# Optimization experiments

Measured on AMD Instinct MI355X. Metric: run time of the kernel, lower is better.

Reference implementation:

```python
import jax, jax.numpy as jnp
import numpy as np

B, S, D = 8, 4, 2048
H, HD = 32, 64
CACHE = 4096


def setup_inputs() -> dict:
    key = jax.random.key(0)
    ks = jax.random.split(key, 8)
    x = jax.random.normal(ks[0], (B, S, D), jnp.float32)
    # rotary frequencies for absolute positions CACHE..CACHE+S-1 (decode step)
    pos = np.arange(CACHE, CACHE + S, dtype=np.float64)[:, None]
    inv = 1.0 / (10000.0 ** (np.arange(0, HD, 2, dtype=np.float64) / HD))
    ang = pos * inv[None, :]
    freqs_cos = jnp.asarray(np.cos(ang), jnp.float32)  # [S, HD//2]
    freqs_sin = jnp.asarray(np.sin(ang), jnp.float32)
    total = CACHE + S
    m = np.zeros((1, 1, S, total), np.float32)
    m[0, 0, :, CACHE:] = np.triu(np.full((S, S), -1e9, np.float32), 1)
    mask = jnp.asarray(m)
    cache_k = jax.random.normal(ks[1], (B, CACHE, H, HD), jnp.float32)
    cache_v = jax.random.normal(ks[2], (B, CACHE, H, HD), jnp.float32)
    scale = 0.02
    wq = scale * jax.random.normal(ks[3], (D, D), jnp.float32)
    wk = scale * jax.random.normal(ks[4], (D, D), jnp.float32)
    wv = scale * jax.random.normal(ks[5], (D, D), jnp.float32)
    wo = scale * jax.random.normal(ks[6], (D, D), jnp.float32)
    return {"x": x, "freqs_cos": freqs_cos, "freqs_sin": freqs_sin,
            "mask": mask, "cache_k": cache_k, "cache_v": cache_v,
            "wq": wq, "wk": wk, "wv": wv, "wo": wo, "start_pos": CACHE}


def _rope(t, cos, sin):
    # t: [B, S, H, HD]; rotate consecutive pairs (complex multiply by e^{i*theta})
    b, s, h, hd = t.shape
    tr = t.reshape(b, s, h, hd // 2, 2)
    t0, t1 = tr[..., 0], tr[..., 1]
    c = cos[None, :, None, :]
    sn = sin[None, :, None, :]
    o0 = t0 * c - t1 * sn
    o1 = t0 * sn + t1 * c
    return jnp.stack([o0, o1], axis=-1).reshape(b, s, h, hd)


def reference(x, freqs_cos, freqs_sin, mask, cache_k, cache_v, wq, wk, wv, wo, start_pos):
    b, s, d = x.shape
    # torch Linear: y = x @ W.T
    xq = (x @ wq.T).reshape(b, s, H, HD)
    xk = (x @ wk.T).reshape(b, s, H, HD)
    xv = (x @ wv.T).reshape(b, s, H, HD)
    xq = _rope(xq, freqs_cos, freqs_sin)
    xk = _rope(xk, freqs_cos, freqs_sin)
    keys = jnp.concatenate([cache_k, xk], axis=1)    # [B, CACHE+S, H, HD]
    values = jnp.concatenate([cache_v, xv], axis=1)
    scale = 1.0 / jnp.sqrt(jnp.asarray(HD, x.dtype))
    scores = jnp.einsum('bqhd,bkhd->bhqk', xq, keys) * scale
    scores = jax.nn.softmax(scores + mask, axis=-1)
    out = jnp.einsum('bhqk,bkhd->bqhd', scores, values).reshape(b, s, d)
    return out @ wo.T
```

## Files before the change

kernel.cpp:

```cpp
#include <hip/hip_runtime.h>

#define DD     2048
#define MM     32
#define HH     32
#define HDIM   64
#define NCACHE 4096
#define KSPLIT 16
#define KR     128
#define NTILE  64
#define LSTR   132

__global__ __launch_bounds__(256) void gemm_partial_k(
    const float* __restrict__ A,
    const float* __restrict__ W0, const float* __restrict__ W1, const float* __restrict__ W2,
    float* __restrict__ partial)
{
    __shared__ float xs[MM][LSTR];
    __shared__ float wsh[NTILE][LSTR];
    const int nt = blockIdx.x, ks = blockIdx.y, wsel = blockIdx.z;
    const float* W = (wsel == 0) ? W0 : (wsel == 1 ? W1 : W2);
    const int k0 = ks * KR, n0 = nt * NTILE, t = threadIdx.x;

#pragma unroll
    for (int p = 0; p < 4; ++p) {
        int idx = t + 256 * p, row = idx >> 5, c4 = (idx & 31) << 2;
        *(float4*)&xs[row][c4] = *(const float4*)(A + (size_t)row * DD + k0 + c4);
    }
#pragma unroll
    for (int p = 0; p < 8; ++p) {
        int idx = t + 256 * p, row = idx >> 5, c4 = (idx & 31) << 2;
        *(float4*)&wsh[row][c4] = *(const float4*)(W + (size_t)(n0 + row) * DD + k0 + c4);
    }
    __syncthreads();

    const int np = t & 31;
    const int m0 = (t >> 5) << 2;
    float acc[4][2] = {{0.f,0.f},{0.f,0.f},{0.f,0.f},{0.f,0.f}};
#pragma unroll 4
    for (int kk = 0; kk < KR; kk += 4) {
        float4 w0 = *(float4*)&wsh[np][kk];
        float4 w1 = *(float4*)&wsh[np + 32][kk];
#pragma unroll
        for (int i = 0; i < 4; ++i) {
            float4 xv = *(float4*)&xs[m0 + i][kk];
            acc[i][0] += xv.x * w0.x + xv.y * w0.y + xv.z * w0.z + xv.w * w0.w;
            acc[i][1] += xv.x * w1.x + xv.y * w1.y + xv.z * w1.z + xv.w * w1.w;
        }
    }
    float* outp = partial + (size_t)(wsel * KSPLIT + ks) * MM * DD;
#pragma unroll
    for (int i = 0; i < 4; ++i) {
        outp[(size_t)(m0 + i) * DD + n0 + np]      = acc[i][0];
        outp[(size_t)(m0 + i) * DD + n0 + 32 + np] = acc[i][1];
    }
}

__global__ __launch_bounds__(256) void reduce_rope_k(
    const float* __restrict__ partial,
    const float* __restrict__ fc, const float* __restrict__ fs,
    float* __restrict__ qkv)
{
    int tid  = blockIdx.x * 256 + threadIdx.x;
    int wsel = tid >> 15;
    int r    = tid & 32767;
    int m    = r >> 10;
    int pr   = r & 1023;
    int n0   = pr << 1;

    const float* p = partial + (size_t)wsel * KSPLIT * MM * DD + (size_t)m * DD + n0;
    float e0 = 0.f, e1 = 0.f;
#pragma unroll
    for (int ksp = 0; ksp < KSPLIT; ++ksp) {
        float2 v = *(const float2*)(p + (size_t)ksp * MM * DD);
        e0 += v.x; e1 += v.y;
    }
    if (wsel < 2) {
        int s = m & 3;
        int i = (n0 & 63) >> 1;
        float c = fc[s * 32 + i], sn = fs[s * 32 + i];
        float o0 = e0 * c - e1 * sn;
        float o1 = e0 * sn + e1 * c;
        e0 = o0; e1 = o1;
    }
    float2 o; o.x = e0; o.y = e1;
    *(float2*)(qkv + (size_t)wsel * MM * DD + (size_t)m * DD + n0) = o;
}

__global__ __launch_bounds__(1024, 4) void attn_k(
    const float* __restrict__ cache_k, const float* __restrict__ cache_v,
    const float* __restrict__ qkv, float* __restrict__ attn_out)
{
    const int b = blockIdx.x >> 5, h = blockIdx.x & 31;
    const int t = threadIdx.x, lane16 = t & 15, grp = t >> 4;
    const int e0 = lane16 << 2;

    float4 q4[4];
#pragma unroll
    for (int q = 0; q < 4; ++q)
        q4[q] = *(const float4*)(qkv + (size_t)(b * 4 + q) * DD + h * HDIM + e0);

    float  l[4]   = {0.f, 0.f, 0.f, 0.f};
    float4 acc[4];
#pragma unroll
    for (int q = 0; q < 4; ++q) { acc[q].x = acc[q].y = acc[q].z = acc[q].w = 0.f; }

    const size_t pstride = (size_t)HH * HDIM;
    const float* kb = cache_k + ((size_t)b * NCACHE * HH + h) * HDIM + e0;
    const float* vb = cache_v + ((size_t)b * NCACHE * HH + h) * HDIM + e0;

    float4 kv = *(const float4*)(kb + (size_t)grp * pstride);
    float4 vv = *(const float4*)(vb + (size_t)grp * pstride);

    for (int it = 0; it < 64; ++it) {
        int pn = grp + (it + 1) * 64;
        if (pn > NCACHE - 1) pn = grp;
        float4 kn = *(const float4*)(kb + (size_t)pn * pstride);
        float4 vn = *(const float4*)(vb + (size_t)pn * pstride);
#pragma unroll
        for (int q = 0; q < 4; ++q) {
            float d = q4[q].x * kv.x + q4[q].y * kv.y + q4[q].z * kv.z + q4[q].w * kv.w;
            d += __shfl_xor(d, 1);
            d += __shfl_xor(d, 2);
            d += __shfl_xor(d, 4);
            d += __shfl_xor(d, 8);
            float pexp = __expf(d * 0.125f);
            l[q] += pexp;
            acc[q].x += pexp * vv.x;
            acc[q].y += pexp * vv.y;
            acc[q].z += pexp * vv.z;
            acc[q].w += pexp * vv.w;
        }
        kv = kn; vv = vn;
    }

    if (grp < 4) {
        const int j = grp;
        float4 k2 = *(const float4*)(qkv + (size_t)MM * DD + (size_t)(b * 4 + j) * DD + h * HDIM + e0);
        float4 v2 = *(const float4*)(qkv + (size_t)2 * MM * DD + (size_t)(b * 4 + j) * DD + h * HDIM + e0);
#pragma unroll
        for (int q = 0; q < 4; ++q) {
            float d = q4[q].x * k2.x + q4[q].y * k2.y + q4[q].z * k2.z + q4[q].w * k2.w;
            d += __shfl_xor(d, 1);
            d += __shfl_xor(d, 2);
            d += __shfl_xor(d, 4);
            d += __shfl_xor(d, 8);
            if (j <= q) {
                float pexp = __expf(d * 0.125f);
                l[q] += pexp;
                acc[q].x += pexp * v2.x;
                acc[q].y += pexp * v2.y;
                acc[q].z += pexp * v2.z;
                acc[q].w += pexp * v2.w;
            }
        }
    }

#pragma unroll
    for (int ofs = 16; ofs < 64; ofs <<= 1) {
#pragma unroll
        for (int q = 0; q < 4; ++q) {
            l[q]     += __shfl_xor(l[q], ofs);
            acc[q].x += __shfl_xor(acc[q].x, ofs);
            acc[q].y += __shfl_xor(acc[q].y, ofs);
            acc[q].z += __shfl_xor(acc[q].z, ofs);
            acc[q].w += __shfl_xor(acc[q].w, ofs);
        }
    }

    __shared__ float lacc[16][4][64];
    __shared__ float lsum[16][4];
    const int w = t >> 6;
    if ((t & 63) < 16) {
#pragma unroll
        for (int q = 0; q < 4; ++q)
            *(float4*)&lacc[w][q][e0] = acc[q];
        if (lane16 == 0) {
#pragma unroll
            for (int q = 0; q < 4; ++q) lsum[w][q] = l[q];
        }
    }
    __syncthreads();
    if (t < 256) {
        int q = t >> 6, e = t & 63;
        float s = 0.f, lt = 0.f;
#pragma unroll
        for (int w2 = 0; w2 < 16; ++w2) { s += lacc[w2][q][e]; lt += lsum[w2][q]; }
        attn_out[(size_t)(b * 4 + q) * DD + h * HDIM + e] = s / lt;
    }
}

__global__ __launch_bounds__(256) void reduce_out_k(
    const float* __restrict__ partial, float* __restrict__ out)
{
    int tid = blockIdx.x * 256 + threadIdx.x;
    int n0 = tid << 1;
    float e0 = 0.f, e1 = 0.f;
#pragma unroll
    for (int ksp = 0; ksp < KSPLIT; ++ksp) {
        float2 v = *(const float2*)(partial + (size_t)ksp * MM * DD + n0);
        e0 += v.x; e1 += v.y;
    }
    float2 o; o.x = e0; o.y = e1;
    *(float2*)(out + n0) = o;
}

extern "C" void kernel_launch(void* const* d_in, const int* in_sizes, int n_in,
                              void* d_out, int out_size, void* d_ws, size_t ws_size,
                              hipStream_t stream)
{
    const float* x       = (const float*)d_in[0];
    const float* fc      = (const float*)d_in[1];
    const float* fs      = (const float*)d_in[2];
    const float* cache_k = (const float*)d_in[4];
    const float* cache_v = (const float*)d_in[5];
    const float* wq      = (const float*)d_in[6];
    const float* wk      = (const float*)d_in[7];
    const float* wv      = (const float*)d_in[8];
    const float* wo      = (const float*)d_in[9];
    float* out = (float*)d_out;

    float* partial1 = (float*)d_ws;
    float* qkv      = partial1 + (size_t)3 * KSPLIT * MM * DD;
    float* attn_o   = qkv + (size_t)3 * MM * DD;
    float* partial2 = partial1;

    gemm_partial_k<<<dim3(32, 16, 3), 256, 0, stream>>>(x, wq, wk, wv, partial1);
    reduce_rope_k<<<384, 256, 0, stream>>>(partial1, fc, fs, qkv);
    attn_k<<<256, 1024, 0, stream>>>(cache_k, cache_v, qkv, attn_o);
    gemm_partial_k<<<dim3(32, 16, 1), 256, 0, stream>>>(attn_o, wo, wo, wo, partial2);
    reduce_out_k<<<128, 256, 0, stream>>>(partial2, out);
}
```

Baseline: 580.6 us.

## Replace split-K partial buffers with atomic accumulation and fuse RoPE into attention

The split-K projection GEMMs now accumulate straight into zero-initialised outputs with atomicAdd, which removes the partial-sum buffers and the two separate reduction kernels. RoPE and the 1/sqrt(d) scale are applied when q and the new k are loaded inside the attention kernel. The GEMM thread mapping changes to 4x4 outputs per thread with the K chunk split across two thread halves, and the attention loop prefetches two cache positions ahead. The cost is atomic contention, nondeterministic summation order, and an extra zeroing kernel.

Result: no change. 578.0 us (-0.4%).

```diff
diff --git a/kernel.cpp b/kernel.cpp
--- a/kernel.cpp
+++ b/kernel.cpp
@@ -10,10 +10,19 @@
 #define NTILE  64
 #define LSTR   132
 
-__global__ __launch_bounds__(256) void gemm_partial_k(
+__global__ __launch_bounds__(256) void zero_k(float4* __restrict__ qkv4,
+                                              float4* __restrict__ out4)
+{
+    int i = blockIdx.x * 256 + threadIdx.x;
+    float4 z; z.x = z.y = z.z = z.w = 0.f;
+    if (i < 16384) out4[i] = z;
+    qkv4[i] = z;
+}
+
+__global__ __launch_bounds__(256) void gemm_atomic_k(
     const float* __restrict__ A,
     const float* __restrict__ W0, const float* __restrict__ W1, const float* __restrict__ W2,
-    float* __restrict__ partial)
+    float* __restrict__ outbase)
 {
     __shared__ float xs[MM][LSTR];
     __shared__ float wsh[NTILE][LSTR];
@@ -33,71 +42,60 @@
     }
     __syncthreads();
 
-    const int np = t & 31;
-    const int m0 = (t >> 5) << 2;
-    float acc[4][2] = {{0.f,0.f},{0.f,0.f},{0.f,0.f},{0.f,0.f}};
+    const int nq = t & 15;
+    const int m0 = ((t >> 4) & 7) << 2;
+    const int kh = (t >> 7) << 6;
+    float acc[4][4];
+#pragma unroll
+    for (int i = 0; i < 4; ++i)
+#pragma unroll
+        for (int j = 0; j < 4; ++j) acc[i][j] = 0.f;
+
 #pragma unroll 4
-    for (int kk = 0; kk < KR; kk += 4) {
-        float4 w0 = *(float4*)&wsh[np][kk];
-        float4 w1 = *(float4*)&wsh[np + 32][kk];
+    for (int kk = kh; kk < kh + 64; kk += 4) {
+        float4 w0 = *(float4*)&wsh[nq][kk];
+        float4 w1 = *(float4*)&wsh[nq + 16][kk];
+        float4 w2 = *(float4*)&wsh[nq + 32][kk];
+        float4 w3 = *(float4*)&wsh[nq + 48][kk];
 #pragma unroll
         for (int i = 0; i < 4; ++i) {
             float4 xv = *(float4*)&xs[m0 + i][kk];
             acc[i][0] += xv.x * w0.x + xv.y * w0.y + xv.z * w0.z + xv.w * w0.w;
             acc[i][1] += xv.x * w1.x + xv.y * w1.y + xv.z * w1.z + xv.w * w1.w;
-        }
-    }
-    float* outp = partial + (size_t)(wsel * KSPLIT + ks) * MM * DD;
-#pragma unroll
-    for (int i = 0; i < 4; ++i) {
-        outp[(size_t)(m0 + i) * DD + n0 + np]      = acc[i][0];
-        outp[(size_t)(m0 + i) * DD + n0 + 32 + np] = acc[i][1];
-    }
-}
-
-__global__ __launch_bounds__(256) void reduce_rope_k(
-    const float* __restrict__ partial,
-    const float* __restrict__ fc, const float* __restrict__ fs,
-    float* __restrict__ qkv)
-{
-    int tid  = blockIdx.x * 256 + threadIdx.x;
-    int wsel = tid >> 15;
-    int r    = tid & 32767;
-    int m    = r >> 10;
-    int pr   = r & 1023;
-    int n0   = pr << 1;
-
-    const float* p = partial + (size_t)wsel * KSPLIT * MM * DD + (size_t)m * DD + n0;
-    float e0 = 0.f, e1 = 0.f;
-#pragma unroll
-    for (int ksp = 0; ksp < KSPLIT; ++ksp) {
-        float2 v = *(const float2*)(p + (size_t)ksp * MM * DD);
-        e0 += v.x; e1 += v.y;
-    }
-    if (wsel < 2) {
-        int s = m & 3;
-        int i = (n0 & 63) >> 1;
-        float c = fc[s * 32 + i], sn = fs[s * 32 + i];
-        float o0 = e0 * c - e1 * sn;
-        float o1 = e0 * sn + e1 * c;
-        e0 = o0; e1 = o1;
-    }
-    float2 o; o.x = e0; o.y = e1;
-    *(float2*)(qkv + (size_t)wsel * MM * DD + (size_t)m * DD + n0) = o;
+            acc[i][2] += xv.x * w2.x + xv.y * w2.y + xv.z * w2.z + xv.w * w2.w;
+            acc[i][3] += xv.x * w3.x + xv.y * w3.y + xv.z * w3.z + xv.w * w3.w;
+        }
+    }
+    float* op = outbase + (size_t)wsel * MM * DD;
+#pragma unroll
+    for (int i = 0; i < 4; ++i)
+#pragma unroll
+        for (int j = 0; j < 4; ++j)
+            atomicAdd(op + (size_t)(m0 + i) * DD + n0 + nq + 16 * j, acc[i][j]);
 }
 
 __global__ __launch_bounds__(1024, 4) void attn_k(
     const float* __restrict__ cache_k, const float* __restrict__ cache_v,
-    const float* __restrict__ qkv, float* __restrict__ attn_out)
+    const float* __restrict__ qkv,
+    const float* __restrict__ fc, const float* __restrict__ fs,
+    float* __restrict__ attn_out)
 {
     const int b = blockIdx.x >> 5, h = blockIdx.x & 31;
     const int t = threadIdx.x, lane16 = t & 15, grp = t >> 4;
     const int e0 = lane16 << 2;
+    const int i0 = e0 >> 1;
 
     float4 q4[4];
 #pragma unroll
-    for (int q = 0; q < 4; ++q)
-        q4[q] = *(const float4*)(qkv + (size_t)(b * 4 + q) * DD + h * HDIM + e0);
+    for (int q = 0; q < 4; ++q) {
+        float4 r = *(const float4*)(qkv + (size_t)(b * 4 + q) * DD + h * HDIM + e0);
+        float c0 = fc[q * 32 + i0],     s0 = fs[q * 32 + i0];
+        float c1 = fc[q * 32 + i0 + 1], s1 = fs[q * 32 + i0 + 1];
+        q4[q].x = (r.x * c0 - r.y * s0) * 0.125f;
+        q4[q].y = (r.x * s0 + r.y * c0) * 0.125f;
+        q4[q].z = (r.z * c1 - r.w * s1) * 0.125f;
+        q4[q].w = (r.z * s1 + r.w * c1) * 0.125f;
+    }
 
     float  l[4]   = {0.f, 0.f, 0.f, 0.f};
     float4 acc[4];
@@ -108,34 +106,52 @@
     const float* kb = cache_k + ((size_t)b * NCACHE * HH + h) * HDIM + e0;
     const float* vb = cache_v + ((size_t)b * NCACHE * HH + h) * HDIM + e0;
 
-    float4 kv = *(const float4*)(kb + (size_t)grp * pstride);
-    float4 vv = *(const float4*)(vb + (size_t)grp * pstride);
-
-    for (int it = 0; it < 64; ++it) {
-        int pn = grp + (it + 1) * 64;
-        if (pn > NCACHE - 1) pn = grp;
-        float4 kn = *(const float4*)(kb + (size_t)pn * pstride);
-        float4 vn = *(const float4*)(vb + (size_t)pn * pstride);
-#pragma unroll
-        for (int q = 0; q < 4; ++q) {
-            float d = q4[q].x * kv.x + q4[q].y * kv.y + q4[q].z * kv.z + q4[q].w * kv.w;
-            d += __shfl_xor(d, 1);
-            d += __shfl_xor(d, 2);
-            d += __shfl_xor(d, 4);
-            d += __shfl_xor(d, 8);
-            float pexp = __expf(d * 0.125f);
-            l[q] += pexp;
-            acc[q].x += pexp * vv.x;
-            acc[q].y += pexp * vv.y;
-            acc[q].z += pexp * vv.z;
-            acc[q].w += pexp * vv.w;
-        }
-        kv = kn; vv = vn;
+    float4 kA = *(const float4*)(kb + (size_t)grp * pstride);
+    float4 vA = *(const float4*)(vb + (size_t)grp * pstride);
+    float4 kB = *(const float4*)(kb + (size_t)(grp + 64) * pstride);
+    float4 vB = *(const float4*)(vb + (size_t)(grp + 64) * pstride);
+
+#define ATT_STEP(KV, VV)                                                      \
+    {                                                                         \
+        _Pragma("unroll")                                                     \
+        for (int q = 0; q < 4; ++q) {                                         \
+            float d = q4[q].x * KV.x + q4[q].y * KV.y +                       \
+                      q4[q].z * KV.z + q4[q].w * KV.w;                        \
+            d += __shfl_xor(d, 1);                                            \
+            d += __shfl_xor(d, 2);                                            \
+            d += __shfl_xor(d, 4);                                            \
+            d += __shfl_xor(d, 8);                                            \
+            float pexp = __expf(d);                                           \
+            l[q] += pexp;                                                     \
+            acc[q].x += pexp * VV.x;                                          \
+            acc[q].y += pexp * VV.y;                                          \
+            acc[q].z += pexp * VV.z;                                          \
+            acc[q].w += pexp * VV.w;                                          \
+        }                                                                     \
+    }
+
+    for (int it = 0; it < 64; it += 2) {
+        int pA = grp + (it + 2) * 64; if (pA > NCACHE - 1) pA = grp;
+        int pB = grp + (it + 3) * 64; if (pB > NCACHE - 1) pB = grp;
+        float4 kC = *(const float4*)(kb + (size_t)pA * pstride);
+        float4 vC = *(const float4*)(vb + (size_t)pA * pstride);
+        float4 kD = *(const float4*)(kb + (size_t)pB * pstride);
+        float4 vD = *(const float4*)(vb + (size_t)pB * pstride);
+        ATT_STEP(kA, vA);
+        ATT_STEP(kB, vB);
+        kA = kC; vA = vC; kB = kD; vB = vD;
     }
 
     if (grp < 4) {
         const int j = grp;
-        float4 k2 = *(const float4*)(qkv + (size_t)MM * DD + (size_t)(b * 4 + j) * DD + h * HDIM + e0);
+        float4 r = *(const float4*)(qkv + (size_t)MM * DD + (size_t)(b * 4 + j) * DD + h * HDIM + e0);
+        float c0 = fc[j * 32 + i0],     s0 = fs[j * 32 + i0];
+        float c1 = fc[j * 32 + i0 + 1], s1 = fs[j * 32 + i0 + 1];
+        float4 k2;
+        k2.x = r.x * c0 - r.y * s0;
+        k2.y = r.x * s0 + r.y * c0;
+        k2.z = r.z * c1 - r.w * s1;
+        k2.w = r.z * s1 + r.w * c1;
         float4 v2 = *(const float4*)(qkv + (size_t)2 * MM * DD + (size_t)(b * 4 + j) * DD + h * HDIM + e0);
 #pragma unroll
         for (int q = 0; q < 4; ++q) {
@@ -145,7 +161,7 @@
             d += __shfl_xor(d, 4);
             d += __shfl_xor(d, 8);
             if (j <= q) {
-                float pexp = __expf(d * 0.125f);
+                float pexp = __expf(d);
                 l[q] += pexp;
                 acc[q].x += pexp * v2.x;
                 acc[q].y += pexp * v2.y;
@@ -187,21 +203,6 @@
         for (int w2 = 0; w2 < 16; ++w2) { s += lacc[w2][q][e]; lt += lsum[w2][q]; }
         attn_out[(size_t)(b * 4 + q) * DD + h * HDIM + e] = s / lt;
     }
-}
-
-__global__ __launch_bounds__(256) void reduce_out_k(
-    const float* __restrict__ partial, float* __restrict__ out)
-{
-    int tid = blockIdx.x * 256 + threadIdx.x;
-    int n0 = tid << 1;
-    float e0 = 0.f, e1 = 0.f;
-#pragma unroll
-    for (int ksp = 0; ksp < KSPLIT; ++ksp) {
-        float2 v = *(const float2*)(partial + (size_t)ksp * MM * DD + n0);
-        e0 += v.x; e1 += v.y;
-    }
-    float2 o; o.x = e0; o.y = e1;
-    *(float2*)(out + n0) = o;
 }
 
 extern "C" void kernel_launch(void* const* d_in, const int* in_sizes, int n_in,
@@ -219,14 +220,11 @@
     const float* wo      = (const float*)d_in[9];
     float* out = (float*)d_out;
 
-    float* partial1 = (float*)d_ws;
-    float* qkv      = partial1 + (size_t)3 * KSPLIT * MM * DD;
-    float* attn_o   = qkv + (size_t)3 * MM * DD;
-    float* partial2 = partial1;
-
-    gemm_partial_k<<<dim3(32, 16, 3), 256, 0, stream>>>(x, wq, wk, wv, partial1);
-    reduce_rope_k<<<384, 256, 0, stream>>>(partial1, fc, fs, qkv);
-    attn_k<<<256, 1024, 0, stream>>>(cache_k, cache_v, qkv, attn_o);
-    gemm_partial_k<<<dim3(32, 16, 1), 256, 0, stream>>>(attn_o, wo, wo, wo, partial2);
-    reduce_out_k<<<128, 256, 0, stream>>>(partial2, out);
-}
+    float* qkv    = (float*)d_ws;
+    float* attn_o = qkv + (size_t)3 * MM * DD;
+
+    zero_k<<<192, 256, 0, stream>>>((float4*)qkv, (float4*)out);
+    gemm_atomic_k<<<dim3(32, 16, 3), 256, 0, stream>>>(x, wq, wk, wv, qkv);
+    attn_k<<<256, 1024, 0, stream>>>(cache_k, cache_v, qkv, fc, fs, attn_o);
+    gemm_atomic_k<<<dim3(32, 16, 1), 256, 0, stream>>>(attn_o, wo, wo, wo, out);
+}
```
